# Kernel optimization log

Hardware: AMD Instinct MI355X
Metric: run time of the kernel (lower is better)

## Reference

```python
import jax, jax.numpy as jnp
import numpy as np

EPSILON = 1e-8
TAU = 0.1

def setup_inputs() -> dict:
    key = jax.random.key(0)
    x = jax.random.normal(key, (8192, 256), dtype=jnp.float32)
    return {"x": x}

def reference(x):
    # L2-normalize rows (torch F.normalize: x / max(||x||, 1e-12))
    norm = jnp.maximum(jnp.linalg.norm(x, axis=1, keepdims=True), 1e-12)
    xn = x / norm
    n = xn.shape[0]
    # pairwise cosine similarity via GEMM (equivalent to broadcast sum in source)
    cos = (xn @ xn.T) / TAU                      # [N, N]
    exp_cos = jnp.exp(cos)
    # zero out diagonal (self-similarity)
    exp_cos = exp_cos * (1.0 - jnp.eye(n, dtype=exp_cos.dtype))
    loss = jnp.log(exp_cos.sum(axis=1) / (n - 1) + EPSILON)
    return jnp.mean(loss)
```

## Files before the change

### kernel.cpp

```cpp
#include <hip/hip_runtime.h>
#include <hip/hip_bf16.h>
#include <math.h>

#define TAU_INV_LOG2E 14.4269504088896340736f
#define EPS 1e-8f

typedef __attribute__((ext_vector_type(8))) short bf16x8;
typedef __attribute__((ext_vector_type(4))) float f32x4;

static __device__ __forceinline__ unsigned short f2bf(float f) {
    unsigned int u = __float_as_uint(f);
    unsigned int r = (u + 0x7fffu + ((u >> 16) & 1u)) >> 16;
    return (unsigned short)r;
}

static __device__ __forceinline__ void glds16(const void* g, void* l) {
    __builtin_amdgcn_global_load_lds(
        (const __attribute__((address_space(1))) unsigned int*)g,
        (__attribute__((address_space(3))) unsigned int*)l,
        16, 0, 0);
}

__global__ __launch_bounds__(256) void normalize_kernel(
    const float* __restrict__ x, unsigned short* __restrict__ xn,
    float* __restrict__ rowsum, int N) {
    const int wave = threadIdx.x >> 6;
    const int lane = threadIdx.x & 63;
    const int row  = blockIdx.x * 4 + wave;
    if (row >= N) return;

    if (threadIdx.x < 4) {
        int rr = blockIdx.x * 4 + threadIdx.x;
        if (rr < N) rowsum[rr] = 0.0f;
    }

    const float4 v = ((const float4*)(x + (size_t)row * 256))[lane];
    float s = v.x * v.x + v.y * v.y + v.z * v.z + v.w * v.w;
    s += __shfl_xor(s, 1);
    s += __shfl_xor(s, 2);
    s += __shfl_xor(s, 4);
    s += __shfl_xor(s, 8);
    s += __shfl_xor(s, 16);
    s += __shfl_xor(s, 32);
    const float norm = fmaxf(sqrtf(s), 1e-12f);
    const float rinv = 1.0f / norm;

    ushort4 o;
    o.x = f2bf(v.x * rinv);
    o.y = f2bf(v.y * rinv);
    o.z = f2bf(v.z * rinv);
    o.w = f2bf(v.w * rinv);
    ((ushort4*)(xn + (size_t)row * 256))[lane] = o;
}

__global__ __launch_bounds__(256, 3) void gemm_exp_rowsum_kernel(
    const unsigned short* __restrict__ xn, float* __restrict__ rowsum, int N) {
    const int D = 256;
    __shared__ unsigned short As[128 * 64];
    __shared__ unsigned short Bs[128 * 64];

    const int tid   = threadIdx.x;
    const int wave  = tid >> 6;
    const int lane  = tid & 63;
    const int waveM = wave >> 1;
    const int waveN = wave & 1;
    const int quad  = lane >> 4;
    const int l16   = lane & 15;

    const int B = N >> 7;
    const int t = blockIdx.x;
    int bi = (int)((2.0 * B + 1.0 -
                    sqrt((2.0 * B + 1.0) * (2.0 * B + 1.0) - 8.0 * (double)t)) * 0.5);
    while (bi > 0 && t < bi * B - (bi * (bi - 1)) / 2) --bi;
    while (t >= (bi + 1) * B - ((bi + 1) * bi) / 2) ++bi;
    const int bj = bi + (t - (bi * B - (bi * (bi - 1)) / 2));
    const bool diag = (bi == bj);

    const int iBase = bi * 128;
    const int jBase = bj * 128;

    f32x4 acc[4][4];
    #pragma unroll
    for (int mt = 0; mt < 4; ++mt)
        #pragma unroll
        for (int nt = 0; nt < 4; ++nt)
            acc[mt][nt] = (f32x4){0.f, 0.f, 0.f, 0.f};

    const int lrow = lane >> 3;
    const int lsw  = (lane & 7) ^ lrow;

    for (int k0 = 0; k0 < D; k0 += 64) {
        #pragma unroll
        for (int it = 0; it < 4; ++it) {
            const int q   = wave * 4 + it;
            const int row = q * 8 + lrow;
            glds16(xn + (size_t)(iBase + row) * D + k0 + lsw * 8, As + q * 512);
            if (!diag)
                glds16(xn + (size_t)(jBase + row) * D + k0 + lsw * 8, Bs + q * 512);
        }
        __syncthreads();

        const unsigned short* Bp = diag ? As : Bs;
        #pragma unroll
        for (int kk = 0; kk < 64; kk += 32) {
            bf16x8 a[4], b[4];
            const int cA = (kk >> 3) + quad;
            #pragma unroll
            for (int tt = 0; tt < 4; ++tt) {
                const int rA = waveM * 64 + tt * 16 + l16;
                a[tt] = *(const bf16x8*)(As + (rA >> 3) * 512 + (rA & 7) * 64 +
                                          ((cA ^ (rA & 7)) * 8));
                const int rB = waveN * 64 + tt * 16 + l16;
                b[tt] = *(const bf16x8*)(Bp + (rB >> 3) * 512 + (rB & 7) * 64 +
                                          ((cA ^ (rB & 7)) * 8));
            }
            #pragma unroll
            for (int mt = 0; mt < 4; ++mt)
                #pragma unroll
                for (int nt = 0; nt < 4; ++nt)
                    acc[mt][nt] = __builtin_amdgcn_mfma_f32_16x16x32_bf16(
                        a[mt], b[nt], acc[mt][nt], 0, 0, 0);
        }
        __syncthreads();
    }

    float rsum[4][4];
    float csum[4] = {0.f, 0.f, 0.f, 0.f};
    #pragma unroll
    for (int mt = 0; mt < 4; ++mt)
        #pragma unroll
        for (int r = 0; r < 4; ++r) rsum[mt][r] = 0.f;

    #pragma unroll
    for (int mt = 0; mt < 4; ++mt) {
        const int gi0 = iBase + waveM * 64 + mt * 16 + quad * 4;
        #pragma unroll
        for (int nt = 0; nt < 4; ++nt) {
            const int gj = jBase + waveN * 64 + nt * 16 + l16;
            #pragma unroll
            for (int r = 0; r < 4; ++r) {
                float e = __builtin_amdgcn_exp2f(acc[mt][nt][r] * TAU_INV_LOG2E);
                if (gi0 + r == gj) e = 0.0f;
                rsum[mt][r] += e;
                csum[nt] += e;
            }
        }
    }
    #pragma unroll
    for (int mt = 0; mt < 4; ++mt) {
        const int gi0 = iBase + waveM * 64 + mt * 16 + quad * 4;
        #pragma unroll
        for (int r = 0; r < 4; ++r) {
            float s = rsum[mt][r];
            s += __shfl_xor(s, 1);
            s += __shfl_xor(s, 2);
            s += __shfl_xor(s, 4);
            s += __shfl_xor(s, 8);
            if (l16 == 0) atomicAdd(&rowsum[gi0 + r], s);
        }
    }
    if (!diag) {
        #pragma unroll
        for (int nt = 0; nt < 4; ++nt) {
            float s = csum[nt];
            s += __shfl_xor(s, 16);
            s += __shfl_xor(s, 32);
            if (quad == 0)
                atomicAdd(&rowsum[jBase + waveN * 64 + nt * 16 + l16], s);
        }
    }
}

__global__ __launch_bounds__(256) void finalize_kernel(
    const float* __restrict__ rowsum, float* __restrict__ out, int N) {
    __shared__ float red[4];
    const float inv = 1.0f / (float)(N - 1);
    float acc = 0.f;
    for (int i = threadIdx.x; i < N; i += 256)
        acc += logf(rowsum[i] * inv + EPS);
    acc += __shfl_xor(acc, 1);
    acc += __shfl_xor(acc, 2);
    acc += __shfl_xor(acc, 4);
    acc += __shfl_xor(acc, 8);
    acc += __shfl_xor(acc, 16);
    acc += __shfl_xor(acc, 32);
    const int wave = threadIdx.x >> 6;
    const int lane = threadIdx.x & 63;
    if (lane == 0) red[wave] = acc;
    __syncthreads();
    if (threadIdx.x == 0) {
        float total = red[0] + red[1] + red[2] + red[3];
        out[0] = total / (float)N;
    }
}

extern "C" void kernel_launch(void* const* d_in, const int* in_sizes, int n_in,
                              void* d_out, int out_size, void* d_ws, size_t ws_size,
                              hipStream_t stream) {
    const float* x = (const float*)d_in[0];
    const int D = 256;
    const int N = in_sizes[0] / D;

    unsigned short* xn = (unsigned short*)d_ws;
    float* rowsum = (float*)((char*)d_ws + (size_t)N * D * sizeof(unsigned short));
    float* out = (float*)d_out;

    normalize_kernel<<<(N + 3) / 4, 256, 0, stream>>>(x, xn, rowsum, N);

    const int B = N / 128;
    const int T = B * (B + 1) / 2;
    gemm_exp_rowsum_kernel<<<T, 256, 0, stream>>>(xn, rowsum, N);

    finalize_kernel<<<1, 256, 0, stream>>>(rowsum, out, N);
}
```

Baseline: 110.3 us.

## Double-buffer LDS tiles in symmetric GEMM and widen finalize reduction

```diff
diff --git a/kernel.cpp b/kernel.cpp
--- a/kernel.cpp
+++ b/kernel.cpp
@@ -53,11 +53,11 @@
     ((ushort4*)(xn + (size_t)row * 256))[lane] = o;
 }
 
-__global__ __launch_bounds__(256, 3) void gemm_exp_rowsum_kernel(
+__global__ __launch_bounds__(256, 2) void gemm_exp_rowsum_kernel(
     const unsigned short* __restrict__ xn, float* __restrict__ rowsum, int N) {
     const int D = 256;
-    __shared__ unsigned short As[128 * 64];
-    __shared__ unsigned short Bs[128 * 64];
+    __shared__ unsigned short As[2][128 * 64];
+    __shared__ unsigned short Bs[2][128 * 64];
 
     const int tid   = threadIdx.x;
     const int wave  = tid >> 6;
@@ -89,18 +89,29 @@
     const int lrow = lane >> 3;
     const int lsw  = (lane & 7) ^ lrow;
 
-    for (int k0 = 0; k0 < D; k0 += 64) {
+    auto stage = [&](int buf, int k0) {
         #pragma unroll
         for (int it = 0; it < 4; ++it) {
             const int q   = wave * 4 + it;
             const int row = q * 8 + lrow;
-            glds16(xn + (size_t)(iBase + row) * D + k0 + lsw * 8, As + q * 512);
+            glds16(xn + (size_t)(iBase + row) * D + k0 + lsw * 8,
+                   &As[buf][q * 512]);
             if (!diag)
-                glds16(xn + (size_t)(jBase + row) * D + k0 + lsw * 8, Bs + q * 512);
-        }
-        __syncthreads();
-
-        const unsigned short* Bp = diag ? As : Bs;
+                glds16(xn + (size_t)(jBase + row) * D + k0 + lsw * 8,
+                       &Bs[buf][q * 512]);
+        }
+    };
+
+    stage(0, 0);
+    __syncthreads();
+
+    #pragma unroll
+    for (int kt = 0; kt < 4; ++kt) {
+        const int cb = kt & 1;
+        if (kt < 3) stage(cb ^ 1, (kt + 1) * 64);
+
+        const unsigned short* Ap = As[cb];
+        const unsigned short* Bp = diag ? As[cb] : Bs[cb];
         #pragma unroll
         for (int kk = 0; kk < 64; kk += 32) {
             bf16x8 a[4], b[4];
@@ -108,7 +119,7 @@
             #pragma unroll
             for (int tt = 0; tt < 4; ++tt) {
                 const int rA = waveM * 64 + tt * 16 + l16;
-                a[tt] = *(const bf16x8*)(As + (rA >> 3) * 512 + (rA & 7) * 64 +
+                a[tt] = *(const bf16x8*)(Ap + (rA >> 3) * 512 + (rA & 7) * 64 +
                                           ((cA ^ (rA & 7)) * 8));
                 const int rB = waveN * 64 + tt * 16 + l16;
                 b[tt] = *(const bf16x8*)(Bp + (rB >> 3) * 512 + (rB & 7) * 64 +
@@ -121,7 +132,7 @@
                     acc[mt][nt] = __builtin_amdgcn_mfma_f32_16x16x32_bf16(
                         a[mt], b[nt], acc[mt][nt], 0, 0, 0);
         }
-        __syncthreads();
+        if (kt < 3) __syncthreads();
     }
 
     float rsum[4][4];
@@ -171,13 +182,17 @@
     }
 }
 
-__global__ __launch_bounds__(256) void finalize_kernel(
+__global__ __launch_bounds__(1024) void finalize_kernel(
     const float* __restrict__ rowsum, float* __restrict__ out, int N) {
-    __shared__ float red[4];
+    __shared__ float red[16];
     const float inv = 1.0f / (float)(N - 1);
     float acc = 0.f;
-    for (int i = threadIdx.x; i < N; i += 256)
-        acc += logf(rowsum[i] * inv + EPS);
+    const float4* r4 = (const float4*)rowsum;
+    for (int i = threadIdx.x; i < (N >> 2); i += 1024) {
+        const float4 v = r4[i];
+        acc += logf(fmaf(v.x, inv, EPS)) + logf(fmaf(v.y, inv, EPS)) +
+               logf(fmaf(v.z, inv, EPS)) + logf(fmaf(v.w, inv, EPS));
+    }
     acc += __shfl_xor(acc, 1);
     acc += __shfl_xor(acc, 2);
     acc += __shfl_xor(acc, 4);
@@ -189,7 +204,9 @@
     if (lane == 0) red[wave] = acc;
     __syncthreads();
     if (threadIdx.x == 0) {
-        float total = red[0] + red[1] + red[2] + red[3];
+        float total = 0.f;
+        #pragma unroll
+        for (int w = 0; w < 16; ++w) total += red[w];
         out[0] = total / (float)N;
     }
 }
@@ -211,5 +228,5 @@
     const int T = B * (B + 1) / 2;
     gemm_exp_rowsum_kernel<<<T, 256, 0, stream>>>(xn, rowsum, N);
 
-    finalize_kernel<<<1, 256, 0, stream>>>(rowsum, out, N);
-}
+    finalize_kernel<<<1, 1024, 0, stream>>>(rowsum, out, N);
+}
```

Result: no change. 111.6 us (+1.2%).
